# Kernel optimization log

Hardware: AMD Instinct MI355X
Metric: run time of the kernel (lower is better)

## Reference

```python
import jax, jax.numpy as jnp
import numpy as np

HIDDEN = 256   # opt.hidden_dim
NHEADS = 8     # forced by .view(bs, nq, -1, 8)
LVLS = 4       # opt.num_feature_levels
NQ = 300       # opt.real_num_queries
BS = 2
LVL_HWS = [(128, 128), (64, 64), (32, 32), (16, 16)]  # ceil((1024/8)/2**l)
OUT = 7        # roi_align output_size
SR = 2         # fixed sampling_ratio (torchvision default -1 is adaptive/data-dependent)
_STARTS = np.cumsum([0] + [h * w for h, w in LVL_HWS]).tolist()


def setup_inputs():
    key = jax.random.key(0)
    ks = jax.random.split(key, 20)
    def rn(i, shape, s=1.0):
        return jax.random.normal(ks[i], shape, jnp.float32) * s
    total = _STARTS[-1]
    memory = rn(0, (BS, total, HIDDEN))
    tgt = rn(1, (BS, NQ, HIDDEN))
    cxcy = jax.random.uniform(ks[2], (BS, NQ, LVLS, 2), jnp.float32)
    ltrb = jax.random.uniform(ks[3], (BS, NQ, LVLS, 4), jnp.float32) * 0.2 + 0.02
    reference = jnp.concatenate([cxcy, ltrb], axis=-1)  # (bs, nq, lvls, 6)
    level_start_index = jnp.array(_STARTS[:LVLS], jnp.int32)
    C4 = HIDDEN // 4
    params = dict(
        p1_w=rn(4, (HIDDEN, C4), 0.05), p1_b=rn(5, (C4,), 0.05),
        p2_w1=rn(6, (C4 * OUT * OUT, 256), 0.02), p2_b1=rn(7, (256,), 0.02),
        p2_w2=rn(8, (256, 512), 0.02), p2_b2=rn(9, (512,), 0.02),
        p2_w3=rn(10, (512, 512), 0.02), p2_b3=rn(11, (512,), 0.02),
        p2_w4=rn(12, (512, NHEADS * 2), 0.02), p2_b4=rn(13, (NHEADS * 2,), 0.02),
        attn1_w=rn(14, (HIDDEN, HIDDEN * NHEADS), 0.02), attn1_b=rn(15, (HIDDEN * NHEADS,), 0.02),
        attn2_w=rn(16, (HIDDEN, 1), 0.05), attn2_b=rn(17, (1,), 0.05))
    return dict(tgt=tgt, memory=memory, reference=reference,
                level_start_index=level_start_index, **params)


def _roi_align(mem2d, boxes):
    """torchvision roi_align, aligned=True, output 7x7, sampling_ratio=SR.
    mem2d: (B,C,H,W); boxes: (B,nq,4) xyxy in feature coords -> (B,nq,C,7,7)."""
    B, C, H, W = mem2d.shape
    nq = boxes.shape[1]
    fl = mem2d.reshape(B, C, H * W)
    x1, y1, x2, y2 = boxes[..., 0], boxes[..., 1], boxes[..., 2], boxes[..., 3]
    sx, sy = x1 - 0.5, y1 - 0.5                      # aligned=True half-pixel offset
    bw, bh = (x2 - x1) / OUT, (y2 - y1) / OUT
    # sample positions: bin pw, subsample ix -> pw + (ix+0.5)/SR  (pw-major order)
    t = (jnp.arange(OUT, dtype=jnp.float32)[:, None]
         + (jnp.arange(SR, dtype=jnp.float32)[None, :] + 0.5) / SR).reshape(-1)  # (S,)
    S = OUT * SR
    xs = sx[..., None] + bw[..., None] * t           # (B,nq,S)
    ys = sy[..., None] + bh[..., None] * t
    yy = jnp.broadcast_to(ys[:, :, :, None], (B, nq, S, S)).reshape(B, -1)
    xx = jnp.broadcast_to(xs[:, :, None, :], (B, nq, S, S)).reshape(B, -1)
    valid = (yy >= -1.0) & (yy <= H) & (xx >= -1.0) & (xx <= W)
    yc = jnp.clip(yy, 0.0, H - 1.0)
    xc = jnp.clip(xx, 0.0, W - 1.0)
    y0 = jnp.clip(jnp.floor(yc), 0.0, H - 2.0)
    x0 = jnp.clip(jnp.floor(xc), 0.0, W - 2.0)
    ly, lx = yc - y0, xc - x0
    y0i, x0i = y0.astype(jnp.int32), x0.astype(jnp.int32)

    def g(yi, xi):
        return jnp.take_along_axis(fl, (yi * W + xi)[:, None, :], axis=2)  # (B,C,P)

    v = (((1 - ly) * (1 - lx))[:, None] * g(y0i, x0i)
         + ((1 - ly) * lx)[:, None] * g(y0i, x0i + 1)
         + (ly * (1 - lx))[:, None] * g(y0i + 1, x0i)
         + (ly * lx)[:, None] * g(y0i + 1, x0i + 1))
    v = v * valid[:, None, :].astype(v.dtype)
    v = v.reshape(B, C, nq, OUT, SR, OUT, SR).mean(axis=(4, 6))  # bin average
    return v.transpose(0, 2, 1, 3, 4)  # (B,nq,C,7,7)


def _grid_sample(feat, gx, gy):
    """F.grid_sample bilinear, padding_mode='zeros', align_corners=False.
    feat: (N,C,H,W); gx,gy: (N,P) in [-1,1] -> (N,C,P)."""
    N, C, H, W = feat.shape
    fl = feat.reshape(N, C, H * W)
    ix = ((gx + 1.0) * W - 1.0) * 0.5
    iy = ((gy + 1.0) * H - 1.0) * 0.5
    x0, y0 = jnp.floor(ix), jnp.floor(iy)
    lx, ly = ix - x0, iy - y0
    out = jnp.zeros((N, C, gx.shape[1]), feat.dtype)
    for dy, dx, w in ((0, 0, (1 - ly) * (1 - lx)), (0, 1, (1 - ly) * lx),
                      (1, 0, ly * (1 - lx)), (1, 1, ly * lx)):
        xi, yi = x0 + dx, y0 + dy
        m = (xi >= 0) & (xi < W) & (yi >= 0) & (yi < H)
        idx = (jnp.clip(yi, 0, H - 1) * W + jnp.clip(xi, 0, W - 1)).astype(jnp.int32)
        out = out + (w * m)[:, None, :] * jnp.take_along_axis(fl, idx[:, None, :], axis=2)
    return out


def _forward(tgt, memory, ref, p1_w, p1_b, p2_w1, p2_b1, p2_w2, p2_b2,
             p2_w3, p2_b3, p2_w4, p2_b4, attn1_w, attn1_b, attn2_w, attn2_b):
    B, nq = tgt.shape[0], tgt.shape[1]
    gate = jax.nn.sigmoid((tgt @ attn1_w + attn1_b).reshape(B, nq, NHEADS, HIDDEN))
    levels = []
    for lvi in range(LVLS):
        h, w = LVL_HWS[lvi]
        s = _STARTS[lvi]
        mem2d = memory[:, s:s + h * w, :].transpose(0, 2, 1).reshape(B, HIDDEN, h, w)
        r = ref[:, :, lvi]                            # (B,nq,6): cx,cy,l,t,r,b
        cx, cy = r[..., 0], r[..., 1]
        x1 = jnp.clip(cx - r[..., 2], 0.0, 1.0) * w
        y1 = jnp.clip(cy - r[..., 3], 0.0, 1.0) * h
        x2 = jnp.clip(cx + r[..., 4], 0.0, 1.0) * w
        y2 = jnp.clip(cy + r[..., 5], 0.0, 1.0) * h
        boxes = jnp.stack([x1, y1, x2, y2], axis=-1)
        roi = _roi_align(mem2d, boxes)                # (B,nq,C,7,7)
        # point1: 1x1 conv + ReLU, then point2 MLP -> per-head sample offsets
        p = jax.nn.relu(jnp.einsum('bqchw,cd->bqdhw', roi, p1_w) + p1_b[:, None, None])
        p = p.reshape(B, nq, -1)
        p = jax.nn.relu(p @ p2_w1 + p2_b1)
        p = jax.nn.relu(p @ p2_w2 + p2_b2)
        p = jax.nn.relu(p @ p2_w3 + p2_b3)
        pts = jnp.tanh(p @ p2_w4 + p2_b4).reshape(B * nq, NHEADS, 2)
        samp = _grid_sample(roi.reshape(B * nq, HIDDEN, OUT, OUT),
                            pts[..., 0], pts[..., 1])           # (B*nq,C,8)
        samp = samp.reshape(B, nq, HIDDEN, NHEADS).transpose(0, 1, 3, 2)  # (B,nq,8,C)
        levels.append(samp * gate)
    qe = jnp.stack(levels, axis=2).reshape(B, nq, LVLS * NHEADS, HIDDEN)
    wgt = jax.nn.softmax((qe @ attn2_w + attn2_b)[..., 0], axis=-1)  # (B,nq,lvls*heads)
    return (qe * wgt[..., None]).sum(axis=-2)  # (B,nq,C)


def reference(tgt, memory, reference, level_start_index, p1_w, p1_b,
              p2_w1, p2_b1, p2_w2, p2_b2, p2_w3, p2_b3, p2_w4, p2_b4,
              attn1_w, attn1_b, attn2_w, attn2_b):
    # level_start_index is consistent with the static LVL_HWS pyramid
    return _forward(tgt, memory, reference, p1_w, p1_b, p2_w1, p2_b1,
                    p2_w2, p2_b2, p2_w3, p2_b3, p2_w4, p2_b4,
                    attn1_w, attn1_b, attn2_w, attn2_b)
```

## Files before the change

### kernel.cpp

```cpp
#include <hip/hip_runtime.h>
#include <hip/hip_bf16.h>

#define NQ     300
#define NH     8
#define HID    256
#define NLVL   4
#define NCELL  49
#define TOTAL  21760

typedef unsigned short ushort_t;
typedef __attribute__((ext_vector_type(8))) short short8;
typedef __attribute__((ext_vector_type(4))) float floatx4;
typedef __attribute__((ext_vector_type(2))) float floatx2;
typedef __attribute__((ext_vector_type(4))) unsigned int uintx4;

__device__ __forceinline__ float bfbits2f(ushort_t u) {
    union { unsigned int i; float f; } x;
    x.i = ((unsigned int)u) << 16;
    return x.f;
}
__device__ __forceinline__ ushort_t f2bfbits(float v) {
    __hip_bfloat16 h = __float2bfloat16(v);
    return *(ushort_t*)&h;
}
__device__ __forceinline__ unsigned int pack2bf(float a, float b) {
    return (unsigned int)f2bfbits(a) | ((unsigned int)f2bfbits(b) << 16);
}
__device__ __forceinline__ void split_bf(float v, ushort_t& hi, ushort_t& lo) {
    __hip_bfloat16 h = __float2bfloat16(v);
    hi = *(ushort_t*)&h;
    float hv = __bfloat162float(h);
    __hip_bfloat16 l = __float2bfloat16(v - hv);
    lo = *(ushort_t*)&l;
}

__device__ __forceinline__ floatx2 pk_fma(floatx2 a, floatx2 b, floatx2 c) {
    floatx2 d;
    asm("v_pk_fma_f32 %0, %1, %2, %3" : "=v"(d) : "v"(a), "v"(b), "v"(c));
    return d;
}
__device__ __forceinline__ floatx2 unpack2(unsigned int u) {
    union { unsigned int i; float f; } lo, hi;
    lo.i = u << 16;
    hi.i = u & 0xffff0000u;
    return (floatx2){lo.f, hi.f};
}
__device__ __forceinline__ uintx4 ld_async_b128(const ushort_t* p) {
    uintx4 d;
    asm volatile("global_load_dwordx4 %0, %1, off" : "=v"(d) : "v"(p));
    return d;
}

struct Box {
    float sx, sy, bw, bh, Wf;
    int W;
    const ushort_t* memb;
};

__device__ __forceinline__ void load_box(const float* __restrict__ refr,
                                         const ushort_t* __restrict__ mem16,
                                         int r, int lvl, int ch, Box& bx) {
    const int lvl_hw[4] = {128, 64, 32, 16};
    const int lvl_s[4]  = {0, 16384, 20480, 21504};
    const int b = r / NQ;
    bx.W  = lvl_hw[lvl];
    bx.Wf = (float)bx.W;
    const float* rp = refr + ((size_t)r * NLVL + lvl) * 6;
    float cx = rp[0], cy = rp[1];
    float dl = rp[2], dt = rp[3], dr = rp[4], db = rp[5];
    float x1 = fminf(fmaxf(cx - dl, 0.f), 1.f) * bx.Wf;
    float y1 = fminf(fmaxf(cy - dt, 0.f), 1.f) * bx.Wf;
    float x2 = fminf(fmaxf(cx + dr, 0.f), 1.f) * bx.Wf;
    float y2 = fminf(fmaxf(cy + db, 0.f), 1.f) * bx.Wf;
    bx.sx = x1 - 0.5f;
    bx.sy = y1 - 0.5f;
    bx.bw = (x2 - x1) * (1.f / 7.f);
    bx.bh = (y2 - y1) * (1.f / 7.f);
    bx.memb = mem16 + ((size_t)b * TOTAL + lvl_s[lvl]) * HID + ch;
}

__device__ __forceinline__ void tsplit_body(const float* __restrict__ W,
                                            ushort_t* __restrict__ TH,
                                            ushort_t* __restrict__ TL,
                                            int K, int N, int kb, int nb,
                                            int perm, int tid, float (*sm)[65]) {
    for (int e = tid; e < 64 * 64; e += 256) {
        int kk = e >> 6, nn = e & 63;
        int kp = kb + kk;
        int ks = perm ? ((kp & 63) * 49 + (kp >> 6)) : kp;
        sm[kk][nn] = W[(size_t)ks * N + nb + nn];
    }
    __syncthreads();
    for (int e = tid; e < 64 * 64; e += 256) {
        int nn = e >> 6, kk = e & 63;
        ushort_t h, l;
        split_bf(sm[kk][nn], h, l);
        size_t o = (size_t)(nb + nn) * K + kb + kk;
        TH[o] = h; TL[o] = l;
    }
}

__global__ __launch_bounds__(256) void k_prep(
    const float* __restrict__ tgt, ushort_t* __restrict__ tgtH, ushort_t* __restrict__ tgtL,
    const float* __restrict__ a1w, ushort_t* __restrict__ a1wTH, ushort_t* __restrict__ a1wTL,
    const float* __restrict__ w1, ushort_t* __restrict__ w1TH, ushort_t* __restrict__ w1TL,
    const float* __restrict__ w2, ushort_t* __restrict__ w2TH, ushort_t* __restrict__ w2TL,
    const float* __restrict__ w3, ushort_t* __restrict__ w3TH, ushort_t* __restrict__ w3TL,
    const float* __restrict__ p1w, ushort_t* __restrict__ p1wTH, ushort_t* __restrict__ p1wTL,
    const float* __restrict__ memory, ushort_t* __restrict__ mem16) {
    __shared__ float sm[64][65];
    const int tid = threadIdx.x;
    int b = blockIdx.x;
    if (b < 600) {
        int i = b * 256 + tid;
        ushort_t h, l;
        split_bf(tgt[i], h, l);
        tgtH[i] = h; tgtL[i] = l;
    } else if (b < 728) {
        b -= 600;
        tsplit_body(a1w, a1wTH, a1wTL, 256, 2048, (b % 4) * 64, (b / 4) * 64, 0, tid, sm);
    } else if (b < 924) {
        b -= 728;
        tsplit_body(w1, w1TH, w1TL, 3136, 256, (b % 49) * 64, (b / 49) * 64, 1, tid, sm);
    } else if (b < 956) {
        b -= 924;
        tsplit_body(w2, w2TH, w2TL, 256, 512, (b % 4) * 64, (b / 4) * 64, 0, tid, sm);
    } else if (b < 1020) {
        b -= 956;
        tsplit_body(w3, w3TH, w3TL, 512, 512, (b % 8) * 64, (b / 8) * 64, 0, tid, sm);
    } else if (b < 1024) {
        b -= 1020;
        tsplit_body(p1w, p1wTH, p1wTL, 256, 64, b * 64, 0, 0, tid, sm);
    } else {
        b -= 1024;
        size_t i = (size_t)b * 256 + tid;
        float4 v = ((const float4*)memory)[i];
        ushort4 o;
        o.x = f2bfbits(v.x); o.y = f2bfbits(v.y);
        o.z = f2bfbits(v.z); o.w = f2bfbits(v.w);
        ((ushort4*)mem16)[i] = o;
    }
}

template <int EPI, int AX>
__global__ __launch_bounds__(256) void k_gmfma(
    const ushort_t* __restrict__ AH, const ushort_t* __restrict__ AL,
    const ushort_t* __restrict__ WH, const ushort_t* __restrict__ WL,
    const float* __restrict__ bias, float* __restrict__ Cf,
    ushort_t* __restrict__ CH, ushort_t* __restrict__ CL,
    int M, int N, int K, int kchunk) {
    __shared__ ushort_t As[AX ? 1 : 2][64][40];
    __shared__ ushort_t Ws[2][64][40];

    const int tid = threadIdx.x;
    const int m0 = blockIdx.x * 64, n0 = blockIdx.y * 64;
    const int wv = tid >> 6, ln = tid & 63;
    const int row = tid >> 2, kc = tid & 3;
    const int gm = min(m0 + row, M - 1);
    const int gn = n0 + row;
    const int arow = wv * 16 + (ln & 15);
    const int koff = (ln >> 4) * 8;

    int kb = 0, ke = K;
    if (EPI == 3) {
        kb = blockIdx.z * kchunk;
        ke = min(K, kb + kchunk);
    }

    floatx4 acc[4];
#pragma unroll
    for (int t = 0; t < 4; ++t) acc[t] = (floatx4){0.f, 0.f, 0.f, 0.f};

    for (int k0 = kb; k0 < ke; k0 += 32) {
        *(uint4*)&As[0][row][kc * 8] = *(const uint4*)(AH + (size_t)gm * K + k0 + kc * 8);
        if constexpr (!AX)
            *(uint4*)&As[AX ? 0 : 1][row][kc * 8] = *(const uint4*)(AL + (size_t)gm * K + k0 + kc * 8);
        *(uint4*)&Ws[0][row][kc * 8] = *(const uint4*)(WH + (size_t)gn * K + k0 + kc * 8);
        *(uint4*)&Ws[1][row][kc * 8] = *(const uint4*)(WL + (size_t)gn * K + k0 + kc * 8);
        __syncthreads();

        short8 aH = *(short8*)&As[0][arow][koff];
        short8 aL = aH;
        if constexpr (!AX) aL = *(short8*)&As[AX ? 0 : 1][arow][koff];
#pragma unroll
        for (int t = 0; t < 4; ++t) {
            short8 wH = *(short8*)&Ws[0][t * 16 + (ln & 15)][koff];
            short8 wL = *(short8*)&Ws[1][t * 16 + (ln & 15)][koff];
            acc[t] = __builtin_amdgcn_mfma_f32_16x16x32_bf16(aH, wH, acc[t], 0, 0, 0);
            acc[t] = __builtin_amdgcn_mfma_f32_16x16x32_bf16(aH, wL, acc[t], 0, 0, 0);
            if constexpr (!AX)
                acc[t] = __builtin_amdgcn_mfma_f32_16x16x32_bf16(aL, wH, acc[t], 0, 0, 0);
        }
        __syncthreads();
    }

    float* Cpart = (EPI == 3) ? Cf + (size_t)blockIdx.z * M * N : Cf;
#pragma unroll
    for (int t = 0; t < 4; ++t) {
        int n = n0 + t * 16 + (ln & 15);
        float bv = (EPI == 3) ? 0.f : bias[n];
#pragma unroll
        for (int reg = 0; reg < 4; ++reg) {
            int m = m0 + wv * 16 + (ln >> 4) * 4 + reg;
            if (m < M) {
                float v = acc[t][reg] + bv;
                if (EPI == 0) {
                    v = fmaxf(v, 0.f);
                    ushort_t h, l;
                    split_bf(v, h, l);
                    CH[(size_t)m * N + n] = h;
                    CL[(size_t)m * N + n] = l;
                } else if (EPI == 1) {
                    Cf[(size_t)m * N + n] = fmaxf(v, 0.f);
                } else if (EPI == 2) {
                    Cf[(size_t)m * N + n] = 1.f / (1.f + expf(-v));
                } else {
                    Cpart[(size_t)m * N + n] = v;
                }
            }
        }
    }
}

template <int EPI, int AX, int KK, int NT>
__global__ __launch_bounds__(256) void k_wres(
    const ushort_t* __restrict__ AH, const ushort_t* __restrict__ AL,
    const ushort_t* __restrict__ WH, const ushort_t* __restrict__ WL,
    const float* __restrict__ bias, float* __restrict__ Cf,
    ushort_t* __restrict__ CH, ushort_t* __restrict__ CL,
    int M, int N, int nbm) {
    constexpr int KC = KK / 8;
    __shared__ ushort_t Wls[2 * NT * KK];

    const int tid = threadIdx.x;
    const int m0 = (blockIdx.x % nbm) * 128;
    const int n0 = (blockIdx.x / nbm) * NT;

    {
        const uint4* sH = (const uint4*)(WH + (size_t)n0 * KK);
        const uint4* sL = (const uint4*)(WL + (size_t)n0 * KK);
        uint4* d = (uint4*)Wls;
        for (int i = tid; i < NT * KC; i += 256) {
            const int nn = i / KC, kk = i % KC;
            const int sw = nn * KC + (kk ^ (nn & 7));
            d[sw] = sH[i];
            d[NT * KC + sw] = sL[i];
        }
    }
    __syncthreads();

    const int wv = tid >> 6, ln = tid & 63;
    const int koff = (ln >> 4) * 8, nidx = ln & 15;
    const size_t a0 = (size_t)min(m0 + wv * 16 + (ln & 15), M - 1) * KK;
    const size_t a1 = (size_t)min(m0 + 64 + wv * 16 + (ln & 15), M - 1) * KK;

    floatx4 acc[2][NT / 16];
#pragma unroll
    for (int s = 0; s < 2; ++s)
#pragma unroll
        for (int t = 0; t < NT / 16; ++t) acc[s][t] = (floatx4){0.f, 0.f, 0.f, 0.f};

    for (int k0 = 0; k0 < KK; k0 += 32) {
        short8 a0H = *(const short8*)(AH + a0 + k0 + koff);
        short8 a1H = *(const short8*)(AH + a1 + k0 + koff);
        short8 a0L = a0H, a1L = a1H;
        if constexpr (!AX) {
            a0L = *(const short8*)(AL + a0 + k0 + koff);
            a1L = *(const short8*)(AL + a1 + k0 + koff);
        }
        const int kc = (k0 + koff) >> 3;
#pragma unroll
        for (int t = 0; t < NT / 16; ++t) {
            const int wrow = t * 16 + nidx;
            const int swr = wrow * KC + (kc ^ (wrow & 7));
            short8 wHf = *(const short8*)((const uint4*)Wls + swr);
            short8 wLf = *(const short8*)((const uint4*)Wls + NT * KC + swr);
            acc[0][t] = __builtin_amdgcn_mfma_f32_16x16x32_bf16(a0H, wHf, acc[0][t], 0, 0, 0);
            acc[0][t] = __builtin_amdgcn_mfma_f32_16x16x32_bf16(a0H, wLf, acc[0][t], 0, 0, 0);
            if constexpr (!AX)
                acc[0][t] = __builtin_amdgcn_mfma_f32_16x16x32_bf16(a0L, wHf, acc[0][t], 0, 0, 0);
            acc[1][t] = __builtin_amdgcn_mfma_f32_16x16x32_bf16(a1H, wHf, acc[1][t], 0, 0, 0);
            acc[1][t] = __builtin_amdgcn_mfma_f32_16x16x32_bf16(a1H, wLf, acc[1][t], 0, 0, 0);
            if constexpr (!AX)
                acc[1][t] = __builtin_amdgcn_mfma_f32_16x16x32_bf16(a1L, wHf, acc[1][t], 0, 0, 0);
        }
    }

#pragma unroll
    for (int s = 0; s < 2; ++s)
#pragma unroll
        for (int t = 0; t < NT / 16; ++t) {
            const int n = n0 + t * 16 + nidx;
            const float bv = bias[n];
#pragma unroll
            for (int reg = 0; reg < 4; ++reg) {
                const int m = m0 + s * 64 + wv * 16 + (ln >> 4) * 4 + reg;
                if (m < M) {
                    float v = acc[s][t][reg] + bv;
                    if constexpr (EPI == 0) {
                        v = fmaxf(v, 0.f);
                        ushort_t h, l;
                        split_bf(v, h, l);
                        CH[(size_t)m * N + n] = h;
                        CL[(size_t)m * N + n] = l;
                    } else if constexpr (EPI == 1) {
                        Cf[(size_t)m * N + n] = fmaxf(v, 0.f);
                    } else {
                        Cf[(size_t)m * N + n] = 1.f / (1.f + expf(-v));
                    }
                }
            }
        }
}

__global__ __launch_bounds__(256) void k_h1red(
    const float* __restrict__ h1p, const float* __restrict__ b1,
    ushort_t* __restrict__ h1H, ushort_t* __restrict__ h1L) {
    const int idx = blockIdx.x * 256 + threadIdx.x;
    const int n = (idx * 4) & 255;
    float4 s = ((const float4*)h1p)[idx];
#pragma unroll
    for (int z = 1; z < 7; ++z) {
        float4 t = ((const float4*)(h1p + (size_t)z * 2400 * 256))[idx];
        s.x += t.x; s.y += t.y; s.z += t.z; s.w += t.w;
    }
    float4 bv = *(const float4*)(b1 + n);
    s.x = fmaxf(s.x + bv.x, 0.f);
    s.y = fmaxf(s.y + bv.y, 0.f);
    s.z = fmaxf(s.z + bv.z, 0.f);
    s.w = fmaxf(s.w + bv.w, 0.f);
    ushort4 H, L;
    split_bf(s.x, H.x, L.x);
    split_bf(s.y, H.y, L.y);
    split_bf(s.z, H.z, L.z);
    split_bf(s.w, H.w, L.w);
    ((ushort4*)h1H)[idx] = H;
    ((ushort4*)h1L)[idx] = L;
}

__global__ __launch_bounds__(256) void k_roi(
    const ushort_t* __restrict__ mem16, const float* __restrict__ refr,
    ushort_t* __restrict__ roi) {
    const int tid  = threadIdx.x;
    const int wave = tid >> 6, lane = tid & 63;
    const int half = lane >> 5;
    const int chv  = (lane & 31) * 8;
    const int bid  = blockIdx.x;

    int lvl, r, klo, khi;
    if (bid < 1200) {
        lvl = 0; r = bid >> 1;
        klo = (bid & 1) ? 13 : 0; khi = (bid & 1) ? 25 : 13;
    } else if (bid < 2400) {
        const int t = bid - 1200;
        lvl = 1; r = t >> 1;
        klo = (t & 1) ? 13 : 0; khi = (t & 1) ? 25 : 13;
    } else if (bid < 3000) {
        lvl = 2; r = bid - 2400; klo = 0; khi = 25;
    } else {
        lvl = 3; r = bid - 3000; klo = 0; khi = 25;
    }
    const int i2 = r * 4 + lvl;

    Box bx;
    load_box(refr, mem16, r, lvl, chv, bx);
    const int rowstride = bx.W * HID;

    ushort_t* rbase = roi + (size_t)i2 * NCELL * HID + chv;

    for (int k = klo + wave; k < khi; k += 4) {
        const int cell = 2 * k + half;
        const int c = (cell < NCELL) ? cell : (NCELL - 1);
        const int ph = c / 7, pw = c % 7;

        uintx4 ld[16];
        float  w[16];
#pragma unroll
        for (int sub = 0; sub < 4; ++sub) {
            const float tys = (float)ph + ((sub >> 1) + 0.5f) * 0.5f;
            const float txs = (float)pw + ((sub & 1) + 0.5f) * 0.5f;
            const float yy = bx.sy + bx.bh * tys;
            const float xx = bx.sx + bx.bw * txs;
            const float vm = (yy >= -1.f && yy <= bx.Wf && xx >= -1.f && xx <= bx.Wf)
                             ? 0.25f : 0.f;
            const float yc  = fminf(fmaxf(yy, 0.f), bx.Wf - 1.f);
            const float xc  = fminf(fmaxf(xx, 0.f), bx.Wf - 1.f);
            const float y0f = fminf(floorf(yc), bx.Wf - 2.f);
            const float x0f = fminf(floorf(xc), bx.Wf - 2.f);
            const float ly = yc - y0f, lx = xc - x0f;
            const int   y0 = (int)y0f, x0 = (int)x0f;
            const ushort_t* p00 = bx.memb + (y0 * bx.W + x0) * HID;
            ld[sub * 4 + 0] = ld_async_b128(p00);
            ld[sub * 4 + 1] = ld_async_b128(p00 + HID);
            ld[sub * 4 + 2] = ld_async_b128(p00 + rowstride);
            ld[sub * 4 + 3] = ld_async_b128(p00 + rowstride + HID);
            const float omy = 1.f - ly, omx = 1.f - lx;
            w[sub * 4 + 0] = vm * omy * omx;
            w[sub * 4 + 1] = vm * omy * lx;
            w[sub * 4 + 2] = vm * ly  * omx;
            w[sub * 4 + 3] = vm * ly  * lx;
        }

        asm volatile("s_waitcnt vmcnt(0)" ::: "memory");
        __builtin_amdgcn_sched_barrier(0);

        floatx2 a01 = (floatx2){0.f, 0.f}, a23 = (floatx2){0.f, 0.f};
        floatx2 a45 = (floatx2){0.f, 0.f}, a67 = (floatx2){0.f, 0.f};
#pragma unroll
        for (int t = 0; t < 16; ++t) {
            const floatx2 wv2 = (floatx2){w[t], w[t]};
            a01 = pk_fma(unpack2(ld[t][0]), wv2, a01);
            a23 = pk_fma(unpack2(ld[t][1]), wv2, a23);
            a45 = pk_fma(unpack2(ld[t][2]), wv2, a45);
            a67 = pk_fma(unpack2(ld[t][3]), wv2, a67);
        }

        if (cell < NCELL) {
            uint4 o;
            o.x = pack2bf(a01.x, a01.y);
            o.y = pack2bf(a23.x, a23.y);
            o.z = pack2bf(a45.x, a45.y);
            o.w = pack2bf(a67.x, a67.y);
            *(uint4*)&rbase[c * HID] = o;
        }
    }
}

__global__ __launch_bounds__(256) void k_fuse(
    const ushort_t* __restrict__ roi, const float* __restrict__ h3,
    const float* __restrict__ w4, const float* __restrict__ b4,
    const float* __restrict__ gate, const float* __restrict__ w,
    const float* __restrict__ bias, float* __restrict__ out) {
    __shared__ float sm_qe[32 * HID];
    __shared__ float sm_pts[64];
    __shared__ float sm_hd[32][4];
    __shared__ float sm_l[32];
    __shared__ float sm_e[32];

    const int tid = threadIdx.x;
    const int r = blockIdx.x;

    float* sm_h3 = sm_qe;
    {
        const float4* src = (const float4*)(h3 + (size_t)r * 4 * 512);
        float4* dst = (float4*)sm_h3;
        for (int i = tid; i < 512; i += 256) dst[i] = src[i];
    }
    __syncthreads();

    {
        const int o = tid >> 2, s = tid & 3;
        const int row = o >> 4, col = o & 15;
        float part = 0.f;
        const int kb = s * 128;
        for (int k = kb; k < kb + 128; ++k)
            part += sm_h3[row * 512 + k] * w4[k * 16 + col];
        part += __shfl_down(part, 2);
        part += __shfl_down(part, 1);
        if (s == 0) sm_pts[row * 16 + col] = tanhf(part + b4[col]);
    }
    __syncthreads();

    if (tid < 32) {
        int lvl = tid >> 3, h = tid & 7;
        float gx = sm_pts[lvl * 16 + h * 2];
        float gy = sm_pts[lvl * 16 + h * 2 + 1];
        float ix = ((gx + 1.f) * 7.f - 1.f) * 0.5f;
        float iy = ((gy + 1.f) * 7.f - 1.f) * 0.5f;
        float x0f = floorf(ix), y0f = floorf(iy);
        sm_hd[tid][0] = x0f;
        sm_hd[tid][1] = y0f;
        sm_hd[tid][2] = ix - x0f;
        sm_hd[tid][3] = iy - y0f;
    }
    __syncthreads();

    const float* grow = gate + (size_t)r * 2048;
#pragma unroll
    for (int j = 0; j < 32; ++j) {
        int lvl = j >> 3, h = j & 7;
        const ushort_t* rbase = roi + ((size_t)r * 4 + lvl) * NCELL * HID;
        float x0f = sm_hd[j][0], y0f = sm_hd[j][1];
        float lx = sm_hd[j][2], ly = sm_hd[j][3];
        int x0 = (int)x0f, y0 = (int)y0f;
        float v = 0.f;
#pragma unroll
        for (int dy = 0; dy < 2; ++dy) {
            int yi = y0 + dy;
            if (yi < 0 || yi >= 7) continue;
            float wy = dy ? ly : 1.f - ly;
#pragma unroll
            for (int dx = 0; dx < 2; ++dx) {
                int xi = x0 + dx;
                if (xi < 0 || xi >= 7) continue;
                float wx = dx ? lx : 1.f - lx;
                v += wy * wx * bfbits2f(rbase[(yi * 7 + xi) * HID + tid]);
            }
        }
        sm_qe[j * HID + tid] = v * grow[h * HID + tid];
    }
    __syncthreads();

    const int j = tid >> 3, sub = tid & 7;
    float part = 0.f;
    const int cbase = sub * 32;
    for (int c = 0; c < 32; ++c) part += sm_qe[j * HID + cbase + c] * w[cbase + c];
    part += __shfl_down(part, 4);
    part += __shfl_down(part, 2);
    part += __shfl_down(part, 1);
    if (sub == 0) sm_l[j] = part + bias[0];
    __syncthreads();
    if (tid < 32) {
        float m = -1e30f;
        for (int i = 0; i < 32; ++i) m = fmaxf(m, sm_l[i]);
        sm_e[tid] = expf(sm_l[tid] - m);
    }
    __syncthreads();
    float denom = 0.f;
    for (int i = 0; i < 32; ++i) denom += sm_e[i];
    float inv = 1.f / denom;
    float acc = 0.f;
    for (int jj = 0; jj < 32; ++jj) acc += sm_qe[jj * HID + tid] * sm_e[jj];
    out[(size_t)r * HID + tid] = acc * inv;
}

extern "C" void kernel_launch(void* const* d_in, const int* in_sizes, int n_in,
                              void* d_out, int out_size, void* d_ws, size_t ws_size,
                              hipStream_t stream) {
    const float* tgt    = (const float*)d_in[0];
    const float* memory = (const float*)d_in[1];
    const float* refr   = (const float*)d_in[2];
    const float* p1w = (const float*)d_in[4];
    const float* p1b = (const float*)d_in[5];
    const float* w1  = (const float*)d_in[6];
    const float* b1  = (const float*)d_in[7];
    const float* w2  = (const float*)d_in[8];
    const float* b2  = (const float*)d_in[9];
    const float* w3  = (const float*)d_in[10];
    const float* b3  = (const float*)d_in[11];
    const float* w4  = (const float*)d_in[12];
    const float* b4  = (const float*)d_in[13];
    const float* a1w = (const float*)d_in[14];
    const float* a1b = (const float*)d_in[15];
    const float* a2w = (const float*)d_in[16];
    const float* a2b = (const float*)d_in[17];
    float* out = (float*)d_out;

    size_t off = 0;
    auto alloc = [&](size_t bytes) {
        void* p = (char*)d_ws + off;
        off += (bytes + 255) & ~(size_t)255;
        return p;
    };
    float*    gate  = (float*)alloc((size_t)600 * 2048 * 4);
    ushort_t* mem16 = (ushort_t*)alloc((size_t)2 * TOTAL * HID * 2);
    ushort_t* roi   = (ushort_t*)alloc((size_t)2400 * NCELL * HID * 2);
    ushort_t* pHb   = (ushort_t*)alloc((size_t)2400 * 3136 * 2);
    ushort_t* pLb   = (ushort_t*)alloc((size_t)2400 * 3136 * 2);
    float*    h1p   = (float*)alloc((size_t)7 * 2400 * 256 * 4);
    ushort_t* h1H   = (ushort_t*)alloc((size_t)2400 * 256 * 2);
    ushort_t* h1L   = (ushort_t*)alloc((size_t)2400 * 256 * 2);
    ushort_t* h2H   = (ushort_t*)alloc((size_t)2400 * 512 * 2);
    ushort_t* h2L   = (ushort_t*)alloc((size_t)2400 * 512 * 2);
    float*    h3    = (float*)alloc((size_t)2400 * 512 * 4);
    ushort_t* tgtH  = (ushort_t*)alloc((size_t)600 * 256 * 2);
    ushort_t* tgtL  = (ushort_t*)alloc((size_t)600 * 256 * 2);
    ushort_t* a1wTH = (ushort_t*)alloc((size_t)2048 * 256 * 2);
    ushort_t* a1wTL = (ushort_t*)alloc((size_t)2048 * 256 * 2);
    ushort_t* w1TH  = (ushort_t*)alloc((size_t)256 * 3136 * 2);
    ushort_t* w1TL  = (ushort_t*)alloc((size_t)256 * 3136 * 2);
    ushort_t* w2TH  = (ushort_t*)alloc((size_t)512 * 256 * 2);
    ushort_t* w2TL  = (ushort_t*)alloc((size_t)512 * 256 * 2);
    ushort_t* w3TH  = (ushort_t*)alloc((size_t)512 * 512 * 2);
    ushort_t* w3TL  = (ushort_t*)alloc((size_t)512 * 512 * 2);
    ushort_t* p1wTH = (ushort_t*)alloc((size_t)64 * 256 * 2);
    ushort_t* p1wTL = (ushort_t*)alloc((size_t)64 * 256 * 2);

    hipLaunchKernelGGL(k_prep, dim3(11904), dim3(256), 0, stream,
                       tgt, tgtH, tgtL, a1w, a1wTH, a1wTL,
                       w1, w1TH, w1TL, w2, w2TH, w2TL, w3, w3TH, w3TL,
                       p1w, p1wTH, p1wTL, memory, mem16);

    hipLaunchKernelGGL((k_wres<2, 0, 256, 64>), dim3(5 * 32), dim3(256), 0, stream,
                       tgtH, tgtL, a1wTH, a1wTL, a1b, gate, (ushort_t*)0, (ushort_t*)0,
                       600, 2048, 5);
    hipLaunchKernelGGL(k_roi, dim3(3600), dim3(256), 0, stream, mem16, refr, roi);
    hipLaunchKernelGGL((k_wres<0, 1, 256, 64>), dim3(919), dim3(256), 0, stream,
                       roi, (ushort_t*)0, p1wTH, p1wTL, p1b, (float*)0, pHb, pLb,
                       2400 * NCELL, 64, 919);
    hipLaunchKernelGGL((k_gmfma<3, 0>), dim3(38, 4, 7), dim3(256), 0, stream,
                       pHb, pLb, w1TH, w1TL, (float*)0, h1p, (ushort_t*)0, (ushort_t*)0,
                       2400, 256, 3136, 448);
    hipLaunchKernelGGL(k_h1red, dim3(600), dim3(256), 0, stream, h1p, b1, h1H, h1L);
    hipLaunchKernelGGL((k_wres<0, 0, 256, 64>), dim3(19 * 8), dim3(256), 0, stream,
                       h1H, h1L, w2TH, w2TL, b2, (float*)0, h2H, h2L, 2400, 512, 19);
    hipLaunchKernelGGL((k_wres<1, 0, 512, 32>), dim3(19 * 16), dim3(256), 0, stream,
                       h2H, h2L, w3TH, w3TL, b3, h3, (ushort_t*)0, (ushort_t*)0,
                       2400, 512, 19);
    hipLaunchKernelGGL(k_fuse, dim3(600), dim3(256), 0, stream,
                       roi, h3, w4, b4, gate, a2w, a2b, out);
}
```

Measured before the change: 337.4 us.

## Replace split-K tiled GEMM with weight-resident LDS kernel for first MLP layer

The generic LDS double-tiled GEMM used for the 3136x256 first MLP layer is replaced by a split-K kernel that loads a whole 32-column by 448-K weight slice (hi and lo) into swizzled shared memory once. A operands are then read straight from global memory into registers, with no per-iteration barriers. Each block now covers 128 rows using two accumulator sets. This removes the per-k-step __syncthreads and the A staging through LDS. In exchange, A fragments are loaded uncoalesced from global, the blocks use more shared memory per block, and the grid shape changes.

```diff
diff --git a/kernel.cpp b/kernel.cpp
--- a/kernel.cpp
+++ b/kernel.cpp
@@ -142,84 +142,74 @@
     }
 }
 
-template <int EPI, int AX>
-__global__ __launch_bounds__(256) void k_gmfma(
+template <int KSTR, int KCH, int NT>
+__global__ __launch_bounds__(256) void k_wskz(
     const ushort_t* __restrict__ AH, const ushort_t* __restrict__ AL,
     const ushort_t* __restrict__ WH, const ushort_t* __restrict__ WL,
-    const float* __restrict__ bias, float* __restrict__ Cf,
-    ushort_t* __restrict__ CH, ushort_t* __restrict__ CL,
-    int M, int N, int K, int kchunk) {
-    __shared__ ushort_t As[AX ? 1 : 2][64][40];
-    __shared__ ushort_t Ws[2][64][40];
+    float* __restrict__ Cf, int M, int N, int nbm) {
+    constexpr int KC = KCH / 8;
+    __shared__ ushort_t Wls[2 * NT * KCH];
 
     const int tid = threadIdx.x;
-    const int m0 = blockIdx.x * 64, n0 = blockIdx.y * 64;
+    const int m0 = (blockIdx.x % nbm) * 128;
+    const int n0 = (blockIdx.x / nbm) * NT;
+    const int kb = blockIdx.z * KCH;
+
+    {
+        uint4* d = (uint4*)Wls;
+        for (int i = tid; i < NT * KC; i += 256) {
+            const int nn = i / KC, kk = i % KC;
+            const int sw = nn * KC + (kk ^ (nn & 7));
+            d[sw] = *(const uint4*)(WH + (size_t)(n0 + nn) * KSTR + kb + kk * 8);
+            d[NT * KC + sw] = *(const uint4*)(WL + (size_t)(n0 + nn) * KSTR + kb + kk * 8);
+        }
+    }
+    __syncthreads();
+
     const int wv = tid >> 6, ln = tid & 63;
-    const int row = tid >> 2, kc = tid & 3;
-    const int gm = min(m0 + row, M - 1);
-    const int gn = n0 + row;
-    const int arow = wv * 16 + (ln & 15);
-    const int koff = (ln >> 4) * 8;
-
-    int kb = 0, ke = K;
-    if (EPI == 3) {
-        kb = blockIdx.z * kchunk;
-        ke = min(K, kb + kchunk);
-    }
-
-    floatx4 acc[4];
-#pragma unroll
-    for (int t = 0; t < 4; ++t) acc[t] = (floatx4){0.f, 0.f, 0.f, 0.f};
-
-    for (int k0 = kb; k0 < ke; k0 += 32) {
-        *(uint4*)&As[0][row][kc * 8] = *(const uint4*)(AH + (size_t)gm * K + k0 + kc * 8);
-        if constexpr (!AX)
-            *(uint4*)&As[AX ? 0 : 1][row][kc * 8] = *(const uint4*)(AL + (size_t)gm * K + k0 + kc * 8);
-        *(uint4*)&Ws[0][row][kc * 8] = *(const uint4*)(WH + (size_t)gn * K + k0 + kc * 8);
-        *(uint4*)&Ws[1][row][kc * 8] = *(const uint4*)(WL + (size_t)gn * K + k0 + kc * 8);
-        __syncthreads();
-
-        short8 aH = *(short8*)&As[0][arow][koff];
-        short8 aL = aH;
-        if constexpr (!AX) aL = *(short8*)&As[AX ? 0 : 1][arow][koff];
-#pragma unroll
-        for (int t = 0; t < 4; ++t) {
-            short8 wH = *(short8*)&Ws[0][t * 16 + (ln & 15)][koff];
-            short8 wL = *(short8*)&Ws[1][t * 16 + (ln & 15)][koff];
-            acc[t] = __builtin_amdgcn_mfma_f32_16x16x32_bf16(aH, wH, acc[t], 0, 0, 0);
-            acc[t] = __builtin_amdgcn_mfma_f32_16x16x32_bf16(aH, wL, acc[t], 0, 0, 0);
-            if constexpr (!AX)
-                acc[t] = __builtin_amdgcn_mfma_f32_16x16x32_bf16(aL, wH, acc[t], 0, 0, 0);
-        }
-        __syncthreads();
-    }
-
-    float* Cpart = (EPI == 3) ? Cf + (size_t)blockIdx.z * M * N : Cf;
-#pragma unroll
-    for (int t = 0; t < 4; ++t) {
-        int n = n0 + t * 16 + (ln & 15);
-        float bv = (EPI == 3) ? 0.f : bias[n];
-#pragma unroll
-        for (int reg = 0; reg < 4; ++reg) {
-            int m = m0 + wv * 16 + (ln >> 4) * 4 + reg;
-            if (m < M) {
-                float v = acc[t][reg] + bv;
-                if (EPI == 0) {
-                    v = fmaxf(v, 0.f);
-                    ushort_t h, l;
-                    split_bf(v, h, l);
-                    CH[(size_t)m * N + n] = h;
-                    CL[(size_t)m * N + n] = l;
-                } else if (EPI == 1) {
-                    Cf[(size_t)m * N + n] = fmaxf(v, 0.f);
-                } else if (EPI == 2) {
-                    Cf[(size_t)m * N + n] = 1.f / (1.f + expf(-v));
-                } else {
-                    Cpart[(size_t)m * N + n] = v;
-                }
+    const int koff = (ln >> 4) * 8, nidx = ln & 15;
+    const size_t a0 = (size_t)min(m0 + wv * 16 + nidx, M - 1) * KSTR + kb;
+    const size_t a1 = (size_t)min(m0 + 64 + wv * 16 + nidx, M - 1) * KSTR + kb;
+
+    floatx4 acc[2][NT / 16];
+#pragma unroll
+    for (int s = 0; s < 2; ++s)
+#pragma unroll
+        for (int t = 0; t < NT / 16; ++t) acc[s][t] = (floatx4){0.f, 0.f, 0.f, 0.f};
+
+    for (int k0 = 0; k0 < KCH; k0 += 32) {
+        short8 a0H = *(const short8*)(AH + a0 + k0 + koff);
+        short8 a0L = *(const short8*)(AL + a0 + k0 + koff);
+        short8 a1H = *(const short8*)(AH + a1 + k0 + koff);
+        short8 a1L = *(const short8*)(AL + a1 + k0 + koff);
+        const int kc = (k0 + koff) >> 3;
+#pragma unroll
+        for (int t = 0; t < NT / 16; ++t) {
+            const int wrow = t * 16 + nidx;
+            const int swr = wrow * KC + (kc ^ (wrow & 7));
+            short8 wHf = *(const short8*)((const uint4*)Wls + swr);
+            short8 wLf = *(const short8*)((const uint4*)Wls + NT * KC + swr);
+            acc[0][t] = __builtin_amdgcn_mfma_f32_16x16x32_bf16(a0H, wHf, acc[0][t], 0, 0, 0);
+            acc[0][t] = __builtin_amdgcn_mfma_f32_16x16x32_bf16(a0H, wLf, acc[0][t], 0, 0, 0);
+            acc[0][t] = __builtin_amdgcn_mfma_f32_16x16x32_bf16(a0L, wHf, acc[0][t], 0, 0, 0);
+            acc[1][t] = __builtin_amdgcn_mfma_f32_16x16x32_bf16(a1H, wHf, acc[1][t], 0, 0, 0);
+            acc[1][t] = __builtin_amdgcn_mfma_f32_16x16x32_bf16(a1H, wLf, acc[1][t], 0, 0, 0);
+            acc[1][t] = __builtin_amdgcn_mfma_f32_16x16x32_bf16(a1L, wHf, acc[1][t], 0, 0, 0);
+        }
+    }
+
+    float* Cp = Cf + (size_t)blockIdx.z * M * N;
+#pragma unroll
+    for (int s = 0; s < 2; ++s)
+#pragma unroll
+        for (int t = 0; t < NT / 16; ++t) {
+            const int n = n0 + t * 16 + nidx;
+#pragma unroll
+            for (int reg = 0; reg < 4; ++reg) {
+                const int m = m0 + s * 64 + wv * 16 + (ln >> 4) * 4 + reg;
+                if (m < M) Cp[(size_t)m * N + n] = acc[s][t][reg];
             }
         }
-    }
 }
 
 template <int EPI, int AX, int KK, int NT>
@@ -588,9 +578,8 @@
     hipLaunchKernelGGL((k_wres<0, 1, 256, 64>), dim3(919), dim3(256), 0, stream,
                        roi, (ushort_t*)0, p1wTH, p1wTL, p1b, (float*)0, pHb, pLb,
                        2400 * NCELL, 64, 919);
-    hipLaunchKernelGGL((k_gmfma<3, 0>), dim3(38, 4, 7), dim3(256), 0, stream,
-                       pHb, pLb, w1TH, w1TL, (float*)0, h1p, (ushort_t*)0, (ushort_t*)0,
-                       2400, 256, 3136, 448);
+    hipLaunchKernelGGL((k_wskz<3136, 448, 32>), dim3(19 * 8, 1, 7), dim3(256), 0, stream,
+                       pHb, pLb, w1TH, w1TL, h1p, 2400, 256, 19);
     hipLaunchKernelGGL(k_h1red, dim3(600), dim3(256), 0, stream, h1p, b1, h1H, h1L);
     hipLaunchKernelGGL((k_wres<0, 0, 256, 64>), dim3(19 * 8), dim3(256), 0, stream,
                        h1H, h1L, w2TH, w2TL, b2, (float*)0, h2H, h2L, 2400, 512, 19);
```

Result: slower. 354.1 us (+5.0%).
